# Kernel tuning notes

Measured on AMD Instinct MI355X. Metric: run time of the kernel, lower is better.

## Reference

```python
import jax, jax.numpy as jnp
import numpy as np

D_MODEL = 1024
N_HEADS = 16
HEAD_DIM = D_MODEL // N_HEADS
B, L, E = 2, 2048, 256


def _linear_params(key, d_out, d_in):
    kw, kb = jax.random.split(key)
    lim = 1.0 / np.sqrt(d_in)
    W = jax.random.uniform(kw, (d_out, d_in), jnp.float32, -lim, lim)
    b = jax.random.uniform(kb, (d_out,), jnp.float32, -lim, lim)
    return W, b


def setup_inputs() -> dict:
    key = jax.random.key(0)
    ks = jax.random.split(key, 10)
    x = jax.random.normal(ks[0], (B, L, D_MODEL), jnp.float32)
    kg_embeds = jax.random.normal(ks[1], (B, E, D_MODEL), jnp.float32)
    Wq, bq = _linear_params(ks[2], D_MODEL, D_MODEL)
    Wk, bk = _linear_params(ks[3], D_MODEL, D_MODEL)
    Wv, bv = _linear_params(ks[4], D_MODEL, D_MODEL)
    Wo, bo = _linear_params(ks[5], D_MODEL, D_MODEL)
    Wkk, bkk = _linear_params(ks[6], D_MODEL, D_MODEL)
    Wkv, bkv = _linear_params(ks[7], D_MODEL, D_MODEL)
    Wg, bg = _linear_params(ks[8], D_MODEL, 2 * D_MODEL)
    return {"x": x, "kg_embeds": kg_embeds,
            "Wq": Wq, "bq": bq, "Wk": Wk, "bk": bk, "Wv": Wv, "bv": bv,
            "Wkk": Wkk, "bkk": bkk, "Wkv": Wkv, "bkv": bkv,
            "Wo": Wo, "bo": bo, "Wg": Wg, "bg": bg}


def _heads(t):
    # [B, S, D] -> [B, H, S, hd]
    Bb, S, _ = t.shape
    return t.reshape(Bb, S, N_HEADS, HEAD_DIM).transpose(0, 2, 1, 3)


def reference(x, kg_embeds, Wq, bq, Wk, bk, Wv, bv, Wkk, bkk, Wkv, bkv, Wo, bo, Wg, bg):
    scale = HEAD_DIM ** -0.5
    q = _heads(x @ Wq.T + bq)                      # [B,H,L,hd]
    k = _heads(x @ Wk.T + bk)
    v = _heads(x @ Wv.T + bv)
    k_kg = _heads(kg_embeds @ Wkk.T + bkk)         # [B,H,E,hd]
    v_kg = _heads(kg_embeds @ Wkv.T + bkv)
    k_aug = jnp.concatenate([k, k_kg], axis=2)     # [B,H,L+E,hd]
    v_aug = jnp.concatenate([v, v_kg], axis=2)
    scores = jnp.einsum('bhld,bhmd->bhlm', q, k_aug) * scale  # [B,H,L,L+E]
    attn = jax.nn.softmax(scores, axis=-1)
    out = jnp.einsum('bhlm,bhmd->bhld', attn, v_aug)           # [B,H,L,hd]
    out = out.transpose(0, 2, 1, 3).reshape(x.shape)            # [B,L,D]
    kg_global = jnp.broadcast_to(kg_embeds.mean(axis=1, keepdims=True), x.shape)
    gate = jax.nn.sigmoid(jnp.concatenate([out, kg_global], axis=-1) @ Wg.T + bg)
    return gate * (out @ Wo.T + bo) + (1.0 - gate) * x
```

## Files before the change

### kernel.cpp

```cpp
#include <hip/hip_runtime.h>
#include <stdint.h>

typedef unsigned short ushort_t;
typedef __attribute__((ext_vector_type(8))) short short8;
typedef __attribute__((ext_vector_type(4))) short short4v;
typedef __attribute__((ext_vector_type(4))) float f32x4;
typedef __attribute__((ext_vector_type(4))) unsigned uintx4;

#define DEV static __device__ __forceinline__

DEV unsigned short f2bf(float f) {
  unsigned u = __builtin_bit_cast(unsigned, f);
  u += 0x7fffu + ((u >> 16) & 1u);
  return (unsigned short)(u >> 16);
}
DEV float bf2f(unsigned short b) {
  return __builtin_bit_cast(float, (unsigned)b << 16);
}

DEV void gl16(const void* g, void* l) {
  __builtin_amdgcn_global_load_lds(
      (__attribute__((address_space(1))) char*)(unsigned long long)g,
      (__attribute__((address_space(3))) char*)(unsigned)(unsigned long long)l,
      16, 0, 0);
}

DEV f32x4 mfma_bf16(short8 a, short8 b, f32x4 c) {
  return __builtin_amdgcn_mfma_f32_16x16x32_bf16(a, b, c, 0, 0, 0);
}

DEV unsigned cvtpk(float lo, float hi) {
  unsigned r;
  asm("v_cvt_pk_bf16_f32 %0, %1, %2" : "=v"(r) : "v"(lo), "v"(hi));
  return r;
}
DEV void swap_net(unsigned& a, unsigned& b) {
  asm("v_permlane32_swap_b32 %0, %1" : "+v"(a), "+v"(b));
  asm("v_permlane16_swap_b32 %0, %1" : "+v"(a), "+v"(b));
}
DEV float redmax4(float x) {
  unsigned a = __builtin_bit_cast(unsigned, x), b = a;
  asm("v_permlane16_swap_b32 %0, %1" : "+v"(a), "+v"(b));
  float y = fmaxf(__builtin_bit_cast(float, a), __builtin_bit_cast(float, b));
  unsigned c = __builtin_bit_cast(unsigned, y), d = c;
  asm("v_permlane32_swap_b32 %0, %1" : "+v"(c), "+v"(d));
  return fmaxf(__builtin_bit_cast(float, c), __builtin_bit_cast(float, d));
}
DEV float lanebcast(float v, int srclane) {
  return __builtin_bit_cast(float,
      __builtin_amdgcn_ds_bpermute(srclane * 4, __builtin_bit_cast(int, v)));
}

__global__ __launch_bounds__(256) void k_cvt_all(
    const float* __restrict__ x, const float* __restrict__ kg,
    const float* __restrict__ Wq, const float* __restrict__ Wk, const float* __restrict__ Wv,
    const float* __restrict__ Wkk, const float* __restrict__ Wkv,
    const float* __restrict__ Wo, const float* __restrict__ Wg,
    ushort_t* __restrict__ xh, ushort_t* __restrict__ kgh,
    ushort_t* __restrict__ WB1, ushort_t* __restrict__ WB2, ushort_t* __restrict__ WB3) {
  const int b = blockIdx.x;
  if (b >= 10752) {
    const int i = (b - 10752) * 256 + threadIdx.x;
    const int r = i >> 8, c = (i & 255) * 4;
    const float4 v = *(const float4*)(Wg + (size_t)r * 2048 + c);
    short4v o;
    o.x = (short)f2bf(v.x); o.y = (short)f2bf(v.y); o.z = (short)f2bf(v.z); o.w = (short)f2bf(v.w);
    *(short4v*)(WB3 + 1048576 + (size_t)r * 1024 + c) = o;
    return;
  }
  const float* src;
  ushort_t* dst;
  int off;
  if (b < 4096)       { src = x;   dst = xh;            off = b; }
  else if (b < 4608)  { src = kg;  dst = kgh;           off = b - 4096; }
  else if (b < 5632)  { src = Wq;  dst = WB1;           off = b - 4608; }
  else if (b < 6656)  { src = Wk;  dst = WB1 + 1048576; off = b - 5632; }
  else if (b < 7680)  { src = Wv;  dst = WB1 + 2097152; off = b - 6656; }
  else if (b < 8704)  { src = Wkk; dst = WB2;           off = b - 7680; }
  else if (b < 9728)  { src = Wkv; dst = WB2 + 1048576; off = b - 8704; }
  else                { src = Wo;  dst = WB3;           off = b - 9728; }
  const int i = off * 1024 + threadIdx.x * 4;
  const float4 v = *(const float4*)(src + i);
  short4v o;
  o.x = (short)f2bf(v.x); o.y = (short)f2bf(v.y); o.z = (short)f2bf(v.z); o.w = (short)f2bf(v.w);
  *(short4v*)(dst + i) = o;
}

__global__ __launch_bounds__(256) void k_kgmean(const float* __restrict__ kg, float* __restrict__ out) {
  const int i = blockIdx.x * 256 + threadIdx.x;
  const int b = i >> 10, d = i & 1023;
  float s = 0.f;
  #pragma unroll 4
  for (int e = 0; e < 256; e++) s += kg[((size_t)b * 256 + e) * 1024 + d];
  out[i] = s * (1.0f / 256.0f);
}

__global__ __launch_bounds__(256) void k_g2(const float* __restrict__ kgm, const float* __restrict__ Wg,
                                            const float* __restrict__ bg, float* __restrict__ g2) {
  const int w = threadIdx.x >> 6, l = threadIdx.x & 63;
  const int idx = blockIdx.x * 4 + w;
  const int b = idx >> 10, n = idx & 1023;
  const float* wr = Wg + (size_t)n * 2048 + 1024;
  const float* mb = kgm + b * 1024;
  float s = 0.f;
  #pragma unroll
  for (int j = 0; j < 16; j++) s += mb[j * 64 + l] * wr[j * 64 + l];
  #pragma unroll
  for (int m = 32; m >= 1; m >>= 1) s += __shfl_xor(s, m);
  if (l == 0) g2[idx] = s + bg[n];
}

template <int MODE>
__global__ __launch_bounds__(512, 2) void k_mm256(
    const ushort_t* __restrict__ A0, const ushort_t* __restrict__ B0,
    const ushort_t* __restrict__ A1, const ushort_t* __restrict__ B1,
    const float* __restrict__ f0, const float* __restrict__ f1, const float* __restrict__ f2,
    const float* __restrict__ f3, const float* __restrict__ f4,
    ushort_t* __restrict__ o0, ushort_t* __restrict__ o1, ushort_t* __restrict__ o2) {
  __shared__ __align__(16) char SHb[131072];
  const int tid = threadIdx.x;
  const int w = tid >> 6, l = tid & 63;
  const int wr = w >> 2, wc = w & 3;
  const int fr = l & 15, fg = l >> 4;

  int m0, n0row, iskg = 0, by;
  if (MODE == 0) {
    const int wg = ((int)blockIdx.x & 7) * 26 + ((int)blockIdx.x >> 3);
    if (wg < 192) { const int bx = wg / 12; by = wg % 12; m0 = bx * 256; }
    else          { const int k = wg - 192; iskg = 1; by = k & 7; m0 = (k >> 3) * 256; }
    n0row = by * 256;
  } else {
    const int wg = ((int)blockIdx.x & 7) * 16 + ((int)blockIdx.x >> 3);
    by = wg & 7; m0 = (wg >> 3) * 256; n0row = by * 256;
  }
  const ushort_t* A = (MODE == 0 && iskg) ? A1 : A0;
  const ushort_t* B = (MODE == 0 && iskg) ? B1 : B0;

  int grow[2], gcb[2];
  #pragma unroll
  for (int j = 0; j < 2; j++) {
    const int beta = j * 512 + tid;
    const int rp = beta >> 3;
    const int u = (beta & 7) ^ (rp & 7);
    grow[j] = 2 * rp + (u >> 2);
    gcb[j] = u & 3;
  }
  const char* gA[2];
  const char* gB[2];
  #pragma unroll
  for (int j = 0; j < 2; j++) {
    gA[j] = (const char*)A + (size_t)(m0 + grow[j]) * 2048 + gcb[j] * 16;
    gB[j] = (const char*)B + (size_t)(n0row + grow[j]) * 2048 + gcb[j] * 16;
  }
  const int dstoff0 = w * 1024 + l * 16;

  auto stage = [&](int s, int kt) {
    char* As = SHb + s * 32768;
    char* Bs = As + 16384;
    const int ko = kt * 64;
    #pragma unroll
    for (int j = 0; j < 2; j++) {
      gl16(gA[j] + ko, As + j * 8192 + dstoff0);
      gl16(gB[j] + ko, Bs + j * 8192 + dstoff0);
    }
  };

  int aoff[8], boff[4];
  #pragma unroll
  for (int i = 0; i < 8; i++) {
    const int row = wr * 128 + i * 16 + fr;
    aoff[i] = (row >> 1) * 128 + ((((row & 1) << 6) | (fg << 4)) ^ (((row >> 1) & 7) << 4));
  }
  #pragma unroll
  for (int j = 0; j < 4; j++) {
    const int row = wc * 64 + j * 16 + fr;
    boff[j] = (row >> 1) * 128 + ((((row & 1) << 6) | (fg << 4)) ^ (((row >> 1) & 7) << 4));
  }

  f32x4 acc[8][4] = {};

  stage(0, 0);
  stage(1, 1);
  int sc = 0, sn2 = 2;
  for (int kt = 0; kt < 32; kt++) {
    if (kt < 31) asm volatile("s_waitcnt vmcnt(4)" ::: "memory");
    else         asm volatile("s_waitcnt vmcnt(0)" ::: "memory");
    __builtin_amdgcn_s_barrier();
    asm volatile("" ::: "memory");
    if (kt <= 29) stage(sn2, kt + 2);
    const char* Ab = SHb + sc * 32768;
    const char* Bb = Ab + 16384;
    short8 af[8], bf[4];
    #pragma unroll
    for (int j = 0; j < 4; j++) bf[j] = *(const short8*)(Bb + boff[j]);
    #pragma unroll
    for (int i = 0; i < 8; i++) af[i] = *(const short8*)(Ab + aoff[i]);
    #pragma unroll
    for (int i = 0; i < 8; i++)
      #pragma unroll
      for (int j = 0; j < 4; j++)
        acc[i][j] = mfma_bf16(af[i], bf[j], acc[i][j]);
    sc++; if (sc == 3) sc = 0;
    sn2++; if (sn2 == 3) sn2 = 0;
  }
  __syncthreads();

  const int sec = (MODE == 0) ? (iskg ? (by >> 2) + 10 : (by >> 2)) : (by >> 2);
  const int nnbase = (by & 3) * 256;
  const bool isV = (MODE == 0) && (sec == 2 || sec == 11);

  if (isV) {
    ushort_t* SHs = (ushort_t*)SHb;
    const float* bV = iskg ? f4 : f2;
    const int bidx = iskg ? (m0 >> 8) : (m0 >> 11);
    const int colbase = iskg ? (2048 + (m0 & 255)) : (m0 & 2047);
    #pragma unroll
    for (int i = 0; i < 8; i++) {
      #pragma unroll
      for (int j = 0; j < 4; j++) {
        const int nl = wc * 64 + j * 16 + fr;
        const int ml0 = wr * 128 + i * 16 + fg * 4;
        const float bb = bV[nnbase + nl];
        short4v pk;
        #pragma unroll
        for (int r = 0; r < 4; r++) pk[r] = (short)f2bf(acc[i][j][r] + bb);
        *(short4v*)(SHs + nl * 256 + (ml0 ^ ((nl & 7) << 3))) = pk;
      }
    }
    __syncthreads();
    const int nl = tid >> 1, mh = tid & 1;
    const int n = nnbase + nl;
    const int h = n >> 6, d = n & 63;
    ushort_t* dst = o2 + ((size_t)(bidx * 16 + h) * 64 + d) * 2304 + colbase + mh * 128;
    const ushort_t* srcr = SHs + nl * 256;
    #pragma unroll
    for (int k2 = 0; k2 < 16; k2++) {
      const int me = (mh * 128 + k2 * 8) ^ ((nl & 7) << 3);
      *(short8*)(dst + k2 * 8) = *(const short8*)(srcr + me);
    }
    return;
  }

  #pragma unroll
  for (int i = 0; i < 8; i++) {
    #pragma unroll
    for (int j = 0; j < 4; j++) {
      const int nn = nnbase + wc * 64 + j * 16 + fr;
      const int h = nn >> 6, d = nn & 63;
      #pragma unroll
      for (int r = 0; r < 4; r++) {
        const int m = m0 + wr * 128 + i * 16 + fg * 4 + r;
        const float v = acc[i][j][r];
        if (MODE == 0) {
          if (sec == 0) {
            const int b = m >> 11, lq = m & 2047;
            o0[((size_t)(b * 16 + h) * 2048 + lq) * 64 + d] = f2bf((v + f0[nn]) * 0.18033688f);
          } else if (sec == 1) {
            const int b = m >> 11, lq = m & 2047;
            o1[((size_t)(b * 16 + h) * 2304 + lq) * 64 + d] = f2bf(v + f1[nn]);
          } else {
            const int b = m >> 8, e = m & 255;
            o1[((size_t)(b * 16 + h) * 2304 + 2048 + e) * 64 + d] = f2bf(v + f3[nn]);
          }
        } else {
          if (sec == 0) o0[(size_t)m * 1024 + nn] = f2bf(v + f0[nn]);
          else          o1[(size_t)m * 1024 + nn] = f2bf(v + f1[(m >> 11) * 1024 + nn]);
        }
      }
    }
  }
}

__global__ __launch_bounds__(256, 4) void k_attn(
    const ushort_t* __restrict__ Qg, const ushort_t* __restrict__ Kg,
    const ushort_t* __restrict__ Vtg, ushort_t* __restrict__ Og) {
  __shared__ __align__(16) ushort_t Ks[2][64 * 64];
  __shared__ __align__(16) ushort_t Vs[2][64 * 64];
  const int tid = threadIdx.x;
  const int w = tid >> 6, l = tid & 63;
  const int fr = l & 15, fg = l >> 4;

  const int id = blockIdx.y * gridDim.x + blockIdx.x;
  const int bh = (id & 7) * 4 + ((id >> 3) >> 5);
  const int q0 = ((id >> 3) & 31) * 64 + w * 16;

  short8 qf[2];
  {
    const short* qrow = (const short*)(Qg + ((size_t)bh * 2048 + q0 + fr) * 64);
    qf[0] = *(const short8*)(qrow + fg * 8);
    qf[1] = *(const short8*)(qrow + 32 + fg * 8);
  }

  constexpr short ONE = 0x3F80;
  const short8 ones = {ONE, ONE, ONE, ONE, ONE, ONE, ONE, ONE};

  f32x4 o[4] = {};
  f32x4 lacc = {};
  float mrun = -1.0e30f;

  const int rsub = tid >> 3;
  const int cS = ((tid & 7) * 16) ^ ((rsub & 7) << 4);
  const char* kbase = (const char*)(Kg + (size_t)bh * 2304 * 64);
  const char* vbase = (const char*)(Vtg + (size_t)bh * 64 * 2304);

  auto stage = [&](int nb, int tile) {
    #pragma unroll
    for (int j = 0; j < 2; j++) {
      const int row = j * 32 + rsub;
      gl16(kbase + (size_t)(tile * 64 + row) * 128 + cS,
           (char*)&Ks[nb][0] + j * 4096 + tid * 16);
      gl16(vbase + (size_t)row * 4608 + tile * 128 + cS,
           (char*)&Vs[nb][0] + j * 4096 + tid * 16);
    }
  };

  stage(0, 0);

  const int rswz = (fr & 7) << 4;

  for (int mt = 0; mt < 36; mt++) {
    __syncthreads();
    if (mt < 35) stage((mt + 1) & 1, mt + 1);

    const char* Kb = (const char*)&Ks[mt & 1][0];
    const char* Vb = (const char*)&Vs[mt & 1][0];

    f32x4 s[4];
    #pragma unroll
    for (int t = 0; t < 4; t++) {
      const int rb = (t * 16 + fr) * 128 + fg * 16;
      const short8 k0 = *(const short8*)(Kb + (rb ^ rswz));
      const short8 k1 = *(const short8*)(Kb + ((rb + 64) ^ rswz));
      f32x4 z = {};
      z = mfma_bf16(k0, qf[0], z);
      z = mfma_bf16(k1, qf[1], z);
      s[t] = z;
    }

    float m = s[0][0];
    #pragma unroll
    for (int t = 0; t < 4; t++)
      #pragma unroll
      for (int r = 0; r < 4; r++) m = fmaxf(m, s[t][r]);
    const float mx = redmax4(m);
    if (__any(mx - mrun > 11.5416f)) {
      const float mn = fmaxf(mrun, mx);
      const float al = __builtin_amdgcn_exp2f(mrun - mn);
      mrun = mn;
      float ab[4];
      #pragma unroll
      for (int r = 0; r < 4; r++) ab[r] = lanebcast(al, fg * 4 + r);
      #pragma unroll
      for (int r = 0; r < 4; r++) {
        lacc[r] *= ab[r];
        #pragma unroll
        for (int dt = 0; dt < 4; dt++) o[dt][r] *= ab[r];
      }
    }
    #pragma unroll
    for (int t = 0; t < 4; t++)
      #pragma unroll
      for (int r = 0; r < 4; r++)
        s[t][r] = __builtin_amdgcn_exp2f(s[t][r] - mrun);

    #pragma unroll
    for (int c = 0; c < 2; c++) {
      unsigned a0 = cvtpk(s[2 * c][0], s[2 * c][1]);
      unsigned b0 = cvtpk(s[2 * c + 1][0], s[2 * c + 1][1]);
      unsigned a1 = cvtpk(s[2 * c][2], s[2 * c][3]);
      unsigned b1 = cvtpk(s[2 * c + 1][2], s[2 * c + 1][3]);
      swap_net(a0, b0);
      swap_net(a1, b1);
      uintx4 u;
      u.x = a0; u.y = a1; u.z = b0; u.w = b1;
      const short8 pf = __builtin_bit_cast(short8, u);
      lacc = mfma_bf16(pf, ones, lacc);
      #pragma unroll
      for (int dt = 0; dt < 4; dt++) {
        const int vb2 = ((dt * 16 + fr) * 128) + fg * 16 + c * 64;
        const short8 vf = *(const short8*)(Vb + (vb2 ^ rswz));
        o[dt] = mfma_bf16(pf, vf, o[dt]);
      }
    }
  }

  const int b = bh >> 4, h = bh & 15;
  #pragma unroll
  for (int r = 0; r < 4; r++) {
    const float inv = 1.0f / lacc[r];
    const int q = q0 + fg * 4 + r;
    ushort_t* orow = Og + ((size_t)b * 2048 + q) * 1024 + h * 64;
    #pragma unroll
    for (int dt = 0; dt < 4; dt++) orow[dt * 16 + fr] = f2bf(o[dt][r] * inv);
  }
}

__global__ __launch_bounds__(256) void k_final(const float* __restrict__ x,
                                               const ushort_t* __restrict__ OUT,
                                               const ushort_t* __restrict__ GL,
                                               float* __restrict__ y) {
  const int i = (blockIdx.x * 256 + threadIdx.x) * 4;
  const float4 xv = *(const float4*)(x + i);
  const short4v ov = *(const short4v*)((const short*)OUT + i);
  const short4v gv = *(const short4v*)((const short*)GL + i);
  float4 r;
  {
    const float o0 = bf2f((unsigned short)ov.x);
    const float g0 = 1.f / (1.f + __expf(-bf2f((unsigned short)gv.x)));
    r.x = xv.x + g0 * (o0 - xv.x);
  }
  {
    const float o1 = bf2f((unsigned short)ov.y);
    const float g1 = 1.f / (1.f + __expf(-bf2f((unsigned short)gv.y)));
    r.y = xv.y + g1 * (o1 - xv.y);
  }
  {
    const float o2 = bf2f((unsigned short)ov.z);
    const float g2 = 1.f / (1.f + __expf(-bf2f((unsigned short)gv.z)));
    r.z = xv.z + g2 * (o2 - xv.z);
  }
  {
    const float o3 = bf2f((unsigned short)ov.w);
    const float g3 = 1.f / (1.f + __expf(-bf2f((unsigned short)gv.w)));
    r.w = xv.w + g3 * (o3 - xv.w);
  }
  *(float4*)(y + i) = r;
}

extern "C" void kernel_launch(void* const* d_in, const int* in_sizes, int n_in,
                              void* d_out, int out_size, void* d_ws, size_t ws_size,
                              hipStream_t stream) {
  (void)in_sizes; (void)n_in; (void)out_size; (void)ws_size;
  const float* x   = (const float*)d_in[0];
  const float* kg  = (const float*)d_in[1];
  const float* Wq  = (const float*)d_in[2];
  const float* bq  = (const float*)d_in[3];
  const float* Wk  = (const float*)d_in[4];
  const float* bk  = (const float*)d_in[5];
  const float* Wv  = (const float*)d_in[6];
  const float* bv  = (const float*)d_in[7];
  const float* Wkk = (const float*)d_in[8];
  const float* bkk = (const float*)d_in[9];
  const float* Wkv = (const float*)d_in[10];
  const float* bkv = (const float*)d_in[11];
  const float* Wo  = (const float*)d_in[12];
  const float* bo  = (const float*)d_in[13];
  const float* Wg  = (const float*)d_in[14];
  const float* bg  = (const float*)d_in[15];
  float* y = (float*)d_out;

  char* ws = (char*)d_ws;
  size_t off = 0;
  auto take = [&](size_t bytes) {
    char* p = ws + off;
    off += (bytes + 255) & ~(size_t)255;
    return p;
  };
  ushort_t* xh   = (ushort_t*)take((size_t)4096 * 1024 * 2);
  ushort_t* kgh  = (ushort_t*)take((size_t)512 * 1024 * 2);
  ushort_t* WB1  = (ushort_t*)take((size_t)3072 * 1024 * 2);
  ushort_t* WB2  = (ushort_t*)take((size_t)2048 * 1024 * 2);
  ushort_t* WB3  = (ushort_t*)take((size_t)2048 * 1024 * 2);
  ushort_t* Qg   = (ushort_t*)take((size_t)32 * 2048 * 64 * 2);
  ushort_t* Kaug = (ushort_t*)take((size_t)32 * 2304 * 64 * 2);
  ushort_t* Vt   = (ushort_t*)take((size_t)32 * 2304 * 64 * 2);
  ushort_t* Og   = (ushort_t*)take((size_t)4096 * 1024 * 2);
  ushort_t* OUTb = (ushort_t*)take((size_t)4096 * 1024 * 2);
  ushort_t* GLb  = (ushort_t*)take((size_t)4096 * 1024 * 2);
  float* kgm     = (float*)take(2048 * 4);
  float* g2      = (float*)take(2048 * 4);

  k_cvt_all<<<11776, 256, 0, stream>>>(x, kg, Wq, Wk, Wv, Wkk, Wkv, Wo, Wg,
                                       xh, kgh, WB1, WB2, WB3);
  k_kgmean<<<8, 256, 0, stream>>>(kg, kgm);
  k_g2<<<512, 256, 0, stream>>>(kgm, Wg, bg, g2);

  k_mm256<0><<<208, 512, 0, stream>>>(xh, WB1, kgh, WB2,
                                      bq, bk, bv, bkk, bkv, Qg, Kaug, Vt);
  k_attn<<<dim3(32, 32), 256, 0, stream>>>(Qg, Kaug, Vt, Og);
  k_mm256<1><<<128, 512, 0, stream>>>(Og, WB3, nullptr, nullptr,
                                      bo, g2, nullptr, nullptr, nullptr, OUTb, GLb, nullptr);
  k_final<<<4096, 256, 0, stream>>>(x, OUTb, GLb, y);
}
```

Before: 201.4 us.

## Shrink projection GEMM tiles to 128x128 with 256-thread blocks for more CTAs

Replaces the 256x256 tile, 512-thread GEMM with a 128x128 tile, 256-thread variant. It also reworks the block-to-tile mapping, the V-transpose epilogue and the section selection. This gives 832 and 512 blocks instead of 208 and 128, which should fill all CUs on a 256-CU part and allow three blocks per CU. It also raises wave priority around the MFMA loop. In exchange each loaded byte is reused less, so more global and LDS traffic is spent per FLOP.

```diff
diff --git a/kernel.cpp b/kernel.cpp
--- a/kernel.cpp
+++ b/kernel.cpp
@@ -111,27 +111,26 @@
 }
 
 template <int MODE>
-__global__ __launch_bounds__(512, 2) void k_mm256(
+__global__ __launch_bounds__(256, 3) void k_mm128(
     const ushort_t* __restrict__ A0, const ushort_t* __restrict__ B0,
     const ushort_t* __restrict__ A1, const ushort_t* __restrict__ B1,
     const float* __restrict__ f0, const float* __restrict__ f1, const float* __restrict__ f2,
     const float* __restrict__ f3, const float* __restrict__ f4,
     ushort_t* __restrict__ o0, ushort_t* __restrict__ o1, ushort_t* __restrict__ o2) {
-  __shared__ __align__(16) char SHb[131072];
+  __shared__ __align__(16) char SHb[49152];
   const int tid = threadIdx.x;
   const int w = tid >> 6, l = tid & 63;
-  const int wr = w >> 2, wc = w & 3;
+  const int wr = w >> 1, wc = w & 1;
   const int fr = l & 15, fg = l >> 4;
 
-  int m0, n0row, iskg = 0, by;
+  int m0, n0, iskg = 0;
   if (MODE == 0) {
-    const int wg = ((int)blockIdx.x & 7) * 26 + ((int)blockIdx.x >> 3);
-    if (wg < 192) { const int bx = wg / 12; by = wg % 12; m0 = bx * 256; }
-    else          { const int k = wg - 192; iskg = 1; by = k & 7; m0 = (k >> 3) * 256; }
-    n0row = by * 256;
+    const int wg = ((int)blockIdx.x & 7) * 104 + ((int)blockIdx.x >> 3);
+    if (wg < 768) { m0 = (wg / 24) * 128; n0 = (wg % 24) * 128; }
+    else          { const int k = wg - 768; iskg = 1; m0 = (k >> 4) * 128; n0 = (k & 15) * 128; }
   } else {
-    const int wg = ((int)blockIdx.x & 7) * 16 + ((int)blockIdx.x >> 3);
-    by = wg & 7; m0 = (wg >> 3) * 256; n0row = by * 256;
+    const int wg = ((int)blockIdx.x & 7) * 64 + ((int)blockIdx.x >> 3);
+    m0 = (wg >> 4) * 128; n0 = (wg & 15) * 128;
   }
   const ushort_t* A = (MODE == 0 && iskg) ? A1 : A0;
   const ushort_t* B = (MODE == 0 && iskg) ? B1 : B0;
@@ -139,7 +138,7 @@
   int grow[2], gcb[2];
   #pragma unroll
   for (int j = 0; j < 2; j++) {
-    const int beta = j * 512 + tid;
+    const int beta = j * 256 + tid;
     const int rp = beta >> 3;
     const int u = (beta & 7) ^ (rp & 7);
     grow[j] = 2 * rp + (u >> 2);
@@ -150,34 +149,30 @@
   #pragma unroll
   for (int j = 0; j < 2; j++) {
     gA[j] = (const char*)A + (size_t)(m0 + grow[j]) * 2048 + gcb[j] * 16;
-    gB[j] = (const char*)B + (size_t)(n0row + grow[j]) * 2048 + gcb[j] * 16;
-  }
-  const int dstoff0 = w * 1024 + l * 16;
+    gB[j] = (const char*)B + (size_t)(n0 + grow[j]) * 2048 + gcb[j] * 16;
+  }
 
   auto stage = [&](int s, int kt) {
-    char* As = SHb + s * 32768;
-    char* Bs = As + 16384;
+    char* As = SHb + s * 16384;
+    char* Bs = As + 8192;
     const int ko = kt * 64;
     #pragma unroll
     for (int j = 0; j < 2; j++) {
-      gl16(gA[j] + ko, As + j * 8192 + dstoff0);
-      gl16(gB[j] + ko, Bs + j * 8192 + dstoff0);
+      gl16(gA[j] + ko, As + j * 4096 + tid * 16);
+      gl16(gB[j] + ko, Bs + j * 4096 + tid * 16);
     }
   };
 
-  int aoff[8], boff[4];
-  #pragma unroll
-  for (int i = 0; i < 8; i++) {
-    const int row = wr * 128 + i * 16 + fr;
-    aoff[i] = (row >> 1) * 128 + ((((row & 1) << 6) | (fg << 4)) ^ (((row >> 1) & 7) << 4));
-  }
-  #pragma unroll
-  for (int j = 0; j < 4; j++) {
-    const int row = wc * 64 + j * 16 + fr;
-    boff[j] = (row >> 1) * 128 + ((((row & 1) << 6) | (fg << 4)) ^ (((row >> 1) & 7) << 4));
-  }
-
-  f32x4 acc[8][4] = {};
+  int aoff[4], boff[4];
+  #pragma unroll
+  for (int i = 0; i < 4; i++) {
+    const int rowa = wr * 64 + i * 16 + fr;
+    aoff[i] = (rowa >> 1) * 128 + ((((rowa & 1) << 6) | (fg << 4)) ^ (((rowa >> 1) & 7) << 4));
+    const int rowb = wc * 64 + i * 16 + fr;
+    boff[i] = (rowb >> 1) * 128 + ((((rowb & 1) << 6) | (fg << 4)) ^ (((rowb >> 1) & 7) << 4));
+  }
+
+  f32x4 acc[4][4] = {};
 
   stage(0, 0);
   stage(1, 1);
@@ -187,27 +182,28 @@
     else         asm volatile("s_waitcnt vmcnt(0)" ::: "memory");
     __builtin_amdgcn_s_barrier();
     asm volatile("" ::: "memory");
-    if (kt <= 29) stage(sn2, kt + 2);
-    const char* Ab = SHb + sc * 32768;
-    const char* Bb = Ab + 16384;
-    short8 af[8], bf[4];
+    if (kt < 30) stage(sn2, kt + 2);
+    const char* Ab = SHb + sc * 16384;
+    const char* Bb = Ab + 8192;
+    short8 af[4], bf[4];
     #pragma unroll
     for (int j = 0; j < 4; j++) bf[j] = *(const short8*)(Bb + boff[j]);
     #pragma unroll
-    for (int i = 0; i < 8; i++) af[i] = *(const short8*)(Ab + aoff[i]);
-    #pragma unroll
-    for (int i = 0; i < 8; i++)
+    for (int i = 0; i < 4; i++) af[i] = *(const short8*)(Ab + aoff[i]);
+    __builtin_amdgcn_s_setprio(1);
+    #pragma unroll
+    for (int i = 0; i < 4; i++)
       #pragma unroll
       for (int j = 0; j < 4; j++)
         acc[i][j] = mfma_bf16(af[i], bf[j], acc[i][j]);
+    __builtin_amdgcn_s_setprio(0);
     sc++; if (sc == 3) sc = 0;
     sn2++; if (sn2 == 3) sn2 = 0;
   }
   __syncthreads();
 
-  const int sec = (MODE == 0) ? (iskg ? (by >> 2) + 10 : (by >> 2)) : (by >> 2);
-  const int nnbase = (by & 3) * 256;
-  const bool isV = (MODE == 0) && (sec == 2 || sec == 11);
+  const int sec = n0 >> 10;
+  const bool isV = (MODE == 0) && ((!iskg && sec == 2) || (iskg && sec == 1));
 
   if (isV) {
     ushort_t* SHs = (ushort_t*)SHb;
@@ -215,52 +211,52 @@
     const int bidx = iskg ? (m0 >> 8) : (m0 >> 11);
     const int colbase = iskg ? (2048 + (m0 & 255)) : (m0 & 2047);
     #pragma unroll
-    for (int i = 0; i < 8; i++) {
+    for (int i = 0; i < 4; i++) {
       #pragma unroll
       for (int j = 0; j < 4; j++) {
         const int nl = wc * 64 + j * 16 + fr;
-        const int ml0 = wr * 128 + i * 16 + fg * 4;
-        const float bb = bV[nnbase + nl];
+        const int ml0 = wr * 64 + i * 16 + fg * 4;
+        const float bb = bV[(n0 & 1023) + nl];
         short4v pk;
         #pragma unroll
         for (int r = 0; r < 4; r++) pk[r] = (short)f2bf(acc[i][j][r] + bb);
-        *(short4v*)(SHs + nl * 256 + (ml0 ^ ((nl & 7) << 3))) = pk;
+        *(short4v*)(SHs + nl * 128 + (ml0 ^ ((nl & 7) << 3))) = pk;
       }
     }
     __syncthreads();
-    const int nl = tid >> 1, mh = tid & 1;
-    const int n = nnbase + nl;
-    const int h = n >> 6, d = n & 63;
-    ushort_t* dst = o2 + ((size_t)(bidx * 16 + h) * 64 + d) * 2304 + colbase + mh * 128;
-    const ushort_t* srcr = SHs + nl * 256;
-    #pragma unroll
-    for (int k2 = 0; k2 < 16; k2++) {
-      const int me = (mh * 128 + k2 * 8) ^ ((nl & 7) << 3);
-      *(short8*)(dst + k2 * 8) = *(const short8*)(srcr + me);
+    const int row = tid >> 1, half = tid & 1;
+    const int h = ((n0 & 1023) >> 6) + (row >> 6);
+    const int d = row & 63;
+    ushort_t* dst = o2 + ((size_t)(bidx * 16 + h) * 64 + d) * 2304 + colbase + half * 64;
+    const ushort_t* srow2 = SHs + row * 128;
+    #pragma unroll
+    for (int k2 = 0; k2 < 8; k2++) {
+      const int me = (half * 64 + k2 * 8) ^ ((row & 7) << 3);
+      *(short8*)(dst + k2 * 8) = *(const short8*)(srow2 + me);
     }
     return;
   }
 
   #pragma unroll
-  for (int i = 0; i < 8; i++) {
+  for (int i = 0; i < 4; i++) {
     #pragma unroll
     for (int j = 0; j < 4; j++) {
-      const int nn = nnbase + wc * 64 + j * 16 + fr;
+      const int nn = (n0 & 1023) + wc * 64 + j * 16 + fr;
       const int h = nn >> 6, d = nn & 63;
       #pragma unroll
       for (int r = 0; r < 4; r++) {
-        const int m = m0 + wr * 128 + i * 16 + fg * 4 + r;
+        const int m = m0 + wr * 64 + i * 16 + fg * 4 + r;
         const float v = acc[i][j][r];
         if (MODE == 0) {
-          if (sec == 0) {
+          if (iskg) {
+            const int b = m >> 8, e = m & 255;
+            o1[((size_t)(b * 16 + h) * 2304 + 2048 + e) * 64 + d] = f2bf(v + f3[nn]);
+          } else if (sec == 0) {
             const int b = m >> 11, lq = m & 2047;
             o0[((size_t)(b * 16 + h) * 2048 + lq) * 64 + d] = f2bf((v + f0[nn]) * 0.18033688f);
-          } else if (sec == 1) {
+          } else {
             const int b = m >> 11, lq = m & 2047;
             o1[((size_t)(b * 16 + h) * 2304 + lq) * 64 + d] = f2bf(v + f1[nn]);
-          } else {
-            const int b = m >> 8, e = m & 255;
-            o1[((size_t)(b * 16 + h) * 2304 + 2048 + e) * 64 + d] = f2bf(v + f3[nn]);
           }
         } else {
           if (sec == 0) o0[(size_t)m * 1024 + nn] = f2bf(v + f0[nn]);
@@ -475,10 +471,10 @@
   k_kgmean<<<8, 256, 0, stream>>>(kg, kgm);
   k_g2<<<512, 256, 0, stream>>>(kgm, Wg, bg, g2);
 
-  k_mm256<0><<<208, 512, 0, stream>>>(xh, WB1, kgh, WB2,
+  k_mm128<0><<<832, 256, 0, stream>>>(xh, WB1, kgh, WB2,
                                       bq, bk, bv, bkk, bkv, Qg, Kaug, Vt);
   k_attn<<<dim3(32, 32), 256, 0, stream>>>(Qg, Kaug, Vt, Og);
-  k_mm256<1><<<128, 512, 0, stream>>>(Og, WB3, nullptr, nullptr,
+  k_mm128<1><<<512, 256, 0, stream>>>(Og, WB3, nullptr, nullptr,
                                       bo, g2, nullptr, nullptr, nullptr, OUTb, GLb, nullptr);
   k_final<<<4096, 256, 0, stream>>>(x, OUTb, GLb, y);
 }
```

Result: faster. 179.4 us (-10.9%).
